# Kernel tuning notes

Measured on AMD Instinct MI355X. Metric: run time of the kernel, lower is better.

Reference implementation:

```python
import jax, jax.numpy as jnp
import numpy as np

N_EMBD = 1024
N_HEAD = 16
HEAD_DIM = N_EMBD // N_HEAD
BLOCK = 2048
BATCH = 2


def setup_inputs() -> dict:
    key = jax.random.key(0)
    ks = jax.random.split(key, 6)
    s_in = 1.0 / np.sqrt(N_EMBD)
    s_hd = 1.0 / np.sqrt(N_EMBD)  # fan-in of c_proj1 is n_head*head_dim = n_embd
    return {
        "x": jax.random.normal(ks[0], (BATCH, BLOCK, N_EMBD), jnp.float32),
        "wq": jax.random.normal(ks[1], (N_EMBD, N_HEAD, HEAD_DIM), jnp.float32) * s_in,
        "wk": jax.random.normal(ks[2], (N_EMBD, N_HEAD, HEAD_DIM), jnp.float32) * s_in,
        "wv": jax.random.normal(ks[3], (N_EMBD, N_HEAD, HEAD_DIM), jnp.float32) * s_in,
        "wp1": jax.random.normal(ks[4], (N_HEAD, HEAD_DIM, N_EMBD), jnp.float32) * s_hd,
        "wp2": jax.random.normal(ks[5], (N_EMBD, N_EMBD), jnp.float32) * s_in,
    }


def reference(x, wq, wk, wv, wp1, wp2):
    # QKV projections: DenseGeneral(features=(H, D), axis=-1), no bias
    q = jnp.einsum('btc,chd->bthd', x, wq)
    k = jnp.einsum('btc,chd->bthd', x, wk)
    v = jnp.einsum('btc,chd->bthd', x, wv)
    scale = HEAD_DIM ** (-0.5)
    wei = jnp.einsum('bqhd,bkhd->bhqk', q, k) * scale  # [B,H,T,T]
    tril = jnp.tril(jnp.ones((BLOCK, BLOCK), dtype=bool))
    wei = jnp.where(tril, wei, -jnp.inf)
    wei = jax.nn.softmax(wei, axis=-1)
    att = jnp.einsum('bhqk,bkhd->bqhd', wei, v)  # [B,T,H,D]
    # c_proj1: DenseGeneral over (-2,-1) -> contract (H,D)
    y = jnp.einsum('bqhd,hdc->bqc', att, wp1)
    # c_proj2: Dense
    out = jnp.einsum('bqc,ce->bqe', y, wp2)
    return out
```

## Files before the change

kernel.cpp:

```cpp
#include <hip/hip_runtime.h>
#include <hip/hip_bf16.h>
#include <stdint.h>

typedef __bf16 bf16;
typedef __bf16 bf16x4 __attribute__((ext_vector_type(4)));
typedef __bf16 bf16x8 __attribute__((ext_vector_type(8)));
typedef float  f32x4  __attribute__((ext_vector_type(4)));

#define MFMA16(a,b,c) __builtin_amdgcn_mfma_f32_16x16x32_bf16((a),(b),(c),0,0,0)

#define TSEQ 2048
#define NE   1024
#define NE3  3072
#define NH   16
#define HD   64
#define MTOK 4096

#if defined(__has_builtin)
#if __has_builtin(__builtin_amdgcn_exp2f)
#define EXP2F(x) __builtin_amdgcn_exp2f(x)
#else
#define EXP2F(x) exp2f(x)
#endif
#else
#define EXP2F(x) exp2f(x)
#endif

__device__ __forceinline__ void gl_lds16(const bf16* g, bf16* l) {
  __builtin_amdgcn_global_load_lds(
      (const __attribute__((address_space(1))) void*)g,
      (__attribute__((address_space(3))) void*)l,
      16, 0, 0);
}

__global__ void k_cast(const float* __restrict__ in, bf16* __restrict__ out, int n4) {
  int i = blockIdx.x * blockDim.x + threadIdx.x;
  if (i < n4) {
    float4 v = reinterpret_cast<const float4*>(in)[i];
    bf16x4 o = { (bf16)v.x, (bf16)v.y, (bf16)v.z, (bf16)v.w };
    reinterpret_cast<bf16x4*>(out)[i] = o;
  }
}

__global__ void k_transpose_all(const float* __restrict__ wq, const float* __restrict__ wk,
                                const float* __restrict__ wv, const float* __restrict__ wp1,
                                const float* __restrict__ wp2,
                                bf16* __restrict__ W3T, bf16* __restrict__ Wp1T,
                                bf16* __restrict__ Wp2T) {
  __shared__ float tile[64][65];
  const int z = blockIdx.z;
  const float* in = (z == 0) ? wq : (z == 1) ? wk : (z == 2) ? wv : (z == 3) ? wp1 : wp2;
  bf16* out = (z < 3) ? (W3T + (size_t)z * 1024 * 1024) : (z == 3 ? Wp1T : Wp2T);
  const int r0 = blockIdx.y * 64, c0 = blockIdx.x * 64;
  const int lc = threadIdx.x & 63, lr0 = threadIdx.x >> 6;
#pragma unroll
  for (int i = 0; i < 16; ++i) {
    int lr = i*4 + lr0;
    tile[lr][lc] = in[(size_t)(r0 + lr) * 1024 + (c0 + lc)];
  }
  __syncthreads();
#pragma unroll
  for (int i = 0; i < 16; ++i) {
    int lr = i*4 + lr0;
    out[(size_t)(c0 + lr) * 1024 + (r0 + lc)] = (bf16)tile[lc][lr];
  }
}

__global__ void k_transpose_v(const bf16* __restrict__ V, bf16* __restrict__ Vt) {
  __shared__ bf16 tile[64][65];
  const int b = blockIdx.z, h = blockIdx.y, t0 = blockIdx.x * 64;
  const int lc = threadIdx.x & 63, lr0 = threadIdx.x >> 6;
#pragma unroll
  for (int i = 0; i < 16; ++i) {
    int lr = i*4 + lr0;
    tile[lr][lc] = V[(size_t)(b*TSEQ + t0 + lr)*NE3 + h*HD + lc];
  }
  __syncthreads();
#pragma unroll
  for (int i = 0; i < 16; ++i) {
    int lr = i*4 + lr0;
    Vt[((size_t)(b*NH + h)*HD + lr)*TSEQ + t0 + lc] = tile[lc][lr];
  }
}

template<int BN, typename OutT>
__global__ __launch_bounds__(256) void k_gemm_bt(const bf16* __restrict__ A,
                                                 const bf16* __restrict__ Bt,
                                                 OutT* __restrict__ C,
                                                 const int M, const int N, const int K) {
  constexpr int NC = BN / 32;
  __shared__ bf16 As[2][128*32];
  __shared__ bf16 Bs[2][BN*32];
  const int tid  = threadIdx.x;
  const int lane = tid & 63;
  const int wave = tid >> 6;
  const int wr = (wave >> 1) * 64;
  const int wc = (wave & 1) * (BN/2);
  const int l15 = lane & 15;
  const int l4  = lane >> 4;
  const int bm = blockIdx.y * 128;
  const int bn = blockIdx.x * BN;

  const int srow = tid >> 2;
  const int scol = ((tid & 3) ^ ((tid >> 3) & 3)) * 8;
  const bf16* ag = A  + (size_t)(bm + srow) * K + scol;
  const bf16* bg = Bt + (size_t)(bn + srow) * K + scol;
  const int kx = (l4 ^ ((l15 >> 1) & 3)) * 8;

  f32x4 acc[4][NC] = {};

  auto stage = [&](int buf, int k0) {
    bf16* al = As[buf] + tid * 8;
    bf16* bl = Bs[buf] + tid * 8;
    gl_lds16(ag + k0,                   al);
    gl_lds16(ag + k0 + (size_t)64 * K,  al + 64*32);
    gl_lds16(bg + k0,                   bl);
    if (BN == 128) gl_lds16(bg + k0 + (size_t)64 * K, bl + 64*32);
  };

  stage(0, 0);
  __syncthreads();
  int cur = 0;
  for (int k0 = 0; k0 < K; k0 += 32) {
    if (k0 + 32 < K) stage(cur ^ 1, k0 + 32);
    bf16x8 af[4], bfr[NC];
#pragma unroll
    for (int m = 0; m < 4; ++m)
      af[m] = *reinterpret_cast<const bf16x8*>(&As[cur][(wr + m*16 + l15)*32 + kx]);
#pragma unroll
    for (int n = 0; n < NC; ++n)
      bfr[n] = *reinterpret_cast<const bf16x8*>(&Bs[cur][(wc + n*16 + l15)*32 + kx]);
#pragma unroll
    for (int m = 0; m < 4; ++m)
#pragma unroll
      for (int n = 0; n < NC; ++n)
        acc[m][n] = MFMA16(af[m], bfr[n], acc[m][n]);
    __syncthreads();
    cur ^= 1;
  }

#pragma unroll
  for (int m = 0; m < 4; ++m) {
    const int row = bm + wr + m*16 + l4*4;
#pragma unroll
    for (int n = 0; n < NC; ++n) {
      const int col = bn + wc + n*16 + l15;
#pragma unroll
      for (int r = 0; r < 4; ++r)
        C[(size_t)(row + r) * N + col] = (OutT)acc[m][n][r];
    }
  }
}

__global__ __launch_bounds__(256) void k_attn(const bf16* __restrict__ QKV,
                                              const bf16* __restrict__ Vt,
                                              bf16* __restrict__ O) {
  __shared__ bf16 Ks[2][2*64*32];
  __shared__ bf16 Vs[2][2*64*32];
  __shared__ bf16 Ps[4][2*32*32];

  const int tid  = threadIdx.x;
  const int lane = tid & 63;
  const int wave = tid >> 6;
  const int l15 = lane & 15;
  const int l4  = lane >> 4;

  const int x  = blockIdx.x;
  const int qb = 15 - (x >> 5);
  const int bh = x & 31;
  const int b  = bh >> 4, h = bh & 15;
  const int qw = qb * 128 + wave * 32;
  const int nt = 2 * qb + 2;

  const bf16* Qb = QKV + (size_t)b*TSEQ*NE3 +        h*HD;
  const bf16* Kb = QKV + (size_t)b*TSEQ*NE3 + 1024 + h*HD;
  const bf16* Vb = Vt  + (size_t)bh*HD*TSEQ;
  bf16* Pw = Ps[wave];

  const float SC = 0.125f * 1.44269504f;
  bf16x8 qf[2][2];
#pragma unroll
  for (int qi = 0; qi < 2; ++qi)
#pragma unroll
    for (int ks = 0; ks < 2; ++ks) {
      bf16x8 qv = *reinterpret_cast<const bf16x8*>(
          &Qb[(size_t)(qw + qi*16 + l15)*NE3 + ks*32 + l4*8]);
#pragma unroll
      for (int j = 0; j < 8; ++j) qv[j] = (bf16)((float)qv[j] * SC);
      qf[qi][ks] = qv;
    }

  f32x4 ot[2][4] = {};
  float m_run[2] = {-1e30f, -1e30f};
  float l_part[2] = {0.f, 0.f};

  const int srow = tid >> 2;
  const int sg   = ((tid & 3) ^ ((tid >> 3) & 3));
  const int swz  = (l4 ^ ((l15 >> 1) & 3)) * 8;

  auto stage = [&](int buf, int t) {
#pragma unroll
    for (int ks = 0; ks < 2; ++ks)
      gl_lds16(&Kb[(size_t)(t*64 + srow)*NE3 + ks*32 + sg*8], &Ks[buf][ks*2048 + tid*8]);
#pragma unroll
    for (int ks = 0; ks < 2; ++ks)
      gl_lds16(&Vb[(size_t)srow*TSEQ + t*64 + ks*32 + sg*8],  &Vs[buf][ks*2048 + tid*8]);
  };

  stage(0, 0);
  __syncthreads();
  int cur = 0;

  for (int t = 0; t < nt; ++t) {
    if (t + 1 < nt) stage(cur ^ 1, t + 1);

    if (t*64 <= qw + 31) {
      f32x4 st[2][4] = {};
#pragma unroll
      for (int kvf = 0; kvf < 4; ++kvf) {
        const int row = kvf*16 + l15;
#pragma unroll
        for (int ks = 0; ks < 2; ++ks) {
          bf16x8 kf = *reinterpret_cast<const bf16x8*>(&Ks[cur][ks*2048 + row*32 + swz]);
          st[0][kvf] = MFMA16(kf, qf[0][ks], st[0][kvf]);
          st[1][kvf] = MFMA16(kf, qf[1][ks], st[1][kvf]);
        }
      }

      const bool maskNeeded = (t*64 + 63 > qw);
#pragma unroll
      for (int qi = 0; qi < 2; ++qi) {
        const int q = qw + qi*16 + l15;
        if (maskNeeded) {
#pragma unroll
          for (int kvf = 0; kvf < 4; ++kvf)
#pragma unroll
            for (int r = 0; r < 4; ++r)
              if (t*64 + kvf*16 + l4*4 + r > q) st[qi][kvf][r] = -1e30f;
        }
        float mx = st[qi][0][0];
#pragma unroll
        for (int kvf = 0; kvf < 4; ++kvf)
#pragma unroll
          for (int r = 0; r < 4; ++r) mx = fmaxf(mx, st[qi][kvf][r]);
        mx = fmaxf(mx, __shfl_xor(mx, 16));
        mx = fmaxf(mx, __shfl_xor(mx, 32));

        if (__any(mx > m_run[qi] + 8.f)) {
          const float mnew = fmaxf(m_run[qi], mx);
          const float corr = EXP2F(m_run[qi] - mnew);
          l_part[qi] *= corr;
#pragma unroll
          for (int n2 = 0; n2 < 4; ++n2) ot[qi][n2] *= corr;
          m_run[qi] = mnew;
        }

        float rs = 0.f;
#pragma unroll
        for (int kvf = 0; kvf < 4; ++kvf) {
          bf16x4 pk;
#pragma unroll
          for (int r = 0; r < 4; ++r) {
            const float p = EXP2F(st[qi][kvf][r] - m_run[qi]);
            rs += p;
            pk[r] = (bf16)p;
          }
          const int gp = (((kvf & 1)*2 + (l4 >> 1)) ^ ((l15 >> 1) & 3));
          *reinterpret_cast<bf16x4*>(
              &Pw[(kvf>>1)*1024 + (qi*16 + l15)*32 + gp*8 + (l4 & 1)*4]) = pk;
        }
        l_part[qi] += rs;
      }

      bf16x8 pa[2][2];
#pragma unroll
      for (int qi = 0; qi < 2; ++qi)
#pragma unroll
        for (int ks = 0; ks < 2; ++ks)
          pa[qi][ks] = *reinterpret_cast<const bf16x8*>(
              &Pw[ks*1024 + (qi*16 + l15)*32 + swz]);
#pragma unroll
      for (int n2 = 0; n2 < 4; ++n2) {
        const int vrow = n2*16 + l15;
#pragma unroll
        for (int ks = 0; ks < 2; ++ks) {
          bf16x8 vf = *reinterpret_cast<const bf16x8*>(&Vs[cur][ks*2048 + vrow*32 + swz]);
          ot[0][n2] = MFMA16(vf, pa[0][ks], ot[0][n2]);
          ot[1][n2] = MFMA16(vf, pa[1][ks], ot[1][n2]);
        }
      }
    }

    __syncthreads();
    cur ^= 1;
  }

#pragma unroll
  for (int qi = 0; qi < 2; ++qi) {
    float l = l_part[qi];
    l += __shfl_xor(l, 16);
    l += __shfl_xor(l, 32);
    const float rl = 1.f / l;
    const size_t row = (size_t)(b*TSEQ + qw + qi*16 + l15);
#pragma unroll
    for (int n2 = 0; n2 < 4; ++n2) {
      bf16x4 ov;
#pragma unroll
      for (int r = 0; r < 4; ++r) ov[r] = (bf16)(ot[qi][n2][r] * rl);
      *reinterpret_cast<bf16x4*>(&O[row*NE + h*HD + n2*16 + l4*4]) = ov;
    }
  }
}

extern "C" void kernel_launch(void* const* d_in, const int* in_sizes, int n_in,
                              void* d_out, int out_size, void* d_ws, size_t ws_size,
                              hipStream_t stream) {
  const float* x   = (const float*)d_in[0];
  const float* wq  = (const float*)d_in[1];
  const float* wk  = (const float*)d_in[2];
  const float* wv  = (const float*)d_in[3];
  const float* wp1 = (const float*)d_in[4];
  const float* wp2 = (const float*)d_in[5];
  float* out = (float*)d_out;

  char* ws = (char*)d_ws;
  const size_t MB = 1024ull * 1024ull;
  bf16* xb   = (bf16*)(ws + 0*MB);
  bf16* W3T  = (bf16*)(ws + 8*MB);
  bf16* wp1T = (bf16*)(ws + 14*MB);
  bf16* wp2T = (bf16*)(ws + 16*MB);
  bf16* QKVb = (bf16*)(ws + 18*MB);
  bf16* Vtb  = (bf16*)(ws + 42*MB);
  bf16* attb = (bf16*)(ws + 50*MB);
  bf16* yb   = (bf16*)(ws + 58*MB);

  k_cast<<<4096, 256, 0, stream>>>(x, xb, MTOK*NE/4);
  k_transpose_all<<<dim3(16, 16, 5), 256, 0, stream>>>(wq, wk, wv, wp1, wp2,
                                                       W3T, wp1T, wp2T);

  k_gemm_bt<128, bf16><<<dim3(24, 32), 256, 0, stream>>>(xb, W3T, QKVb, MTOK, NE3, NE);

  k_transpose_v<<<dim3(TSEQ/64, NH, 2), 256, 0, stream>>>(QKVb + 2048, Vtb);

  k_attn<<<dim3(512), 256, 0, stream>>>(QKVb, Vtb, attb);

  k_gemm_bt<64, bf16 ><<<dim3(16, 32), 256, 0, stream>>>(attb, wp1T, yb,  MTOK, NE, NE);
  k_gemm_bt<64, float><<<dim3(16, 32), 256, 0, stream>>>(yb,   wp2T, out, MTOK, NE, NE);
}
```

Baseline: 142.3 us.

## Fold output projections into one weight, rebalance causal attention, swizzle GEMM tiles

Precomputes the product of the two output projection weights on device, so the attention output needs one GEMM instead of two. Attention blocks shrink to two waves, and each block handles a paired short and long causal chunk so work per block evens out. GEMM tiles are remapped in groups of eight to improve cache locality. The exp2 builtin is swapped for exp2f. Folding the weights adds a small 1024^3 GEMM per call and changes bf16 rounding.

```diff
diff --git a/kernel.cpp b/kernel.cpp
--- a/kernel.cpp
+++ b/kernel.cpp
@@ -16,15 +16,7 @@
 #define HD   64
 #define MTOK 4096
 
-#if defined(__has_builtin)
-#if __has_builtin(__builtin_amdgcn_exp2f)
-#define EXP2F(x) __builtin_amdgcn_exp2f(x)
-#else
 #define EXP2F(x) exp2f(x)
-#endif
-#else
-#define EXP2F(x) exp2f(x)
-#endif
 
 __device__ __forceinline__ void gl_lds16(const bf16* g, bf16* l) {
   __builtin_amdgcn_global_load_lds(
@@ -43,14 +35,12 @@
 }
 
 __global__ void k_transpose_all(const float* __restrict__ wq, const float* __restrict__ wk,
-                                const float* __restrict__ wv, const float* __restrict__ wp1,
-                                const float* __restrict__ wp2,
-                                bf16* __restrict__ W3T, bf16* __restrict__ Wp1T,
-                                bf16* __restrict__ Wp2T) {
+                                const float* __restrict__ wv, const float* __restrict__ wp2,
+                                bf16* __restrict__ W3T, bf16* __restrict__ Wp2T) {
   __shared__ float tile[64][65];
   const int z = blockIdx.z;
-  const float* in = (z == 0) ? wq : (z == 1) ? wk : (z == 2) ? wv : (z == 3) ? wp1 : wp2;
-  bf16* out = (z < 3) ? (W3T + (size_t)z * 1024 * 1024) : (z == 3 ? Wp1T : Wp2T);
+  const float* in = (z == 0) ? wq : (z == 1) ? wk : (z == 2) ? wv : wp2;
+  bf16* out = (z < 3) ? (W3T + (size_t)z * 1024 * 1024) : Wp2T;
   const int r0 = blockIdx.y * 64, c0 = blockIdx.x * 64;
   const int lc = threadIdx.x & 63, lr0 = threadIdx.x >> 6;
 #pragma unroll
@@ -98,8 +88,12 @@
   const int wc = (wave & 1) * (BN/2);
   const int l15 = lane & 15;
   const int l4  = lane >> 4;
-  const int bm = blockIdx.y * 128;
-  const int bn = blockIdx.x * BN;
+
+  const int nwg = gridDim.x * gridDim.y;
+  int id = blockIdx.y * gridDim.x + blockIdx.x;
+  id = (id & 7) * (nwg >> 3) + (id >> 3);
+  const int bm = (id / gridDim.x) * 128;
+  const int bn = (id % gridDim.x) * BN;
 
   const int srow = tid >> 2;
   const int scol = ((tid & 3) ^ ((tid >> 3) & 3)) * 8;
@@ -152,12 +146,12 @@
   }
 }
 
-__global__ __launch_bounds__(256) void k_attn(const bf16* __restrict__ QKV,
+__global__ __launch_bounds__(128) void k_attn(const bf16* __restrict__ QKV,
                                               const bf16* __restrict__ Vt,
                                               bf16* __restrict__ O) {
   __shared__ bf16 Ks[2][2*64*32];
   __shared__ bf16 Vs[2][2*64*32];
-  __shared__ bf16 Ps[4][2*32*32];
+  __shared__ bf16 Ps[2][2*32*32];
 
   const int tid  = threadIdx.x;
   const int lane = tid & 63;
@@ -166,11 +160,9 @@
   const int l4  = lane >> 4;
 
   const int x  = blockIdx.x;
-  const int qb = 15 - (x >> 5);
+  const int p  = x >> 5;
   const int bh = x & 31;
   const int b  = bh >> 4, h = bh & 15;
-  const int qw = qb * 128 + wave * 32;
-  const int nt = 2 * qb + 2;
 
   const bf16* Qb = QKV + (size_t)b*TSEQ*NE3 +        h*HD;
   const bf16* Kb = QKV + (size_t)b*TSEQ*NE3 + 1024 + h*HD;
@@ -178,43 +170,62 @@
   bf16* Pw = Ps[wave];
 
   const float SC = 0.125f * 1.44269504f;
-  bf16x8 qf[2][2];
-#pragma unroll
-  for (int qi = 0; qi < 2; ++qi)
-#pragma unroll
-    for (int ks = 0; ks < 2; ++ks) {
-      bf16x8 qv = *reinterpret_cast<const bf16x8*>(
-          &Qb[(size_t)(qw + qi*16 + l15)*NE3 + ks*32 + l4*8]);
-#pragma unroll
-      for (int j = 0; j < 8; ++j) qv[j] = (bf16)((float)qv[j] * SC);
-      qf[qi][ks] = qv;
-    }
-
-  f32x4 ot[2][4] = {};
-  float m_run[2] = {-1e30f, -1e30f};
-  float l_part[2] = {0.f, 0.f};
-
-  const int srow = tid >> 2;
-  const int sg   = ((tid & 3) ^ ((tid >> 3) & 3));
-  const int swz  = (l4 ^ ((l15 >> 1) & 3)) * 8;
+  const int swz = (l4 ^ ((l15 >> 1) & 3)) * 8;
+  const int sr = tid >> 2;
+  const int sg = tid & 3;
 
   auto stage = [&](int buf, int t) {
 #pragma unroll
     for (int ks = 0; ks < 2; ++ks)
-      gl_lds16(&Kb[(size_t)(t*64 + srow)*NE3 + ks*32 + sg*8], &Ks[buf][ks*2048 + tid*8]);
+#pragma unroll
+      for (int half = 0; half < 2; ++half) {
+        const int r = half*32 + sr;
+        const int g = sg ^ ((r >> 1) & 3);
+        gl_lds16(&Kb[(size_t)(t*64 + r)*NE3 + ks*32 + g*8],
+                 &Ks[buf][ks*2048 + half*1024 + tid*8]);
+      }
 #pragma unroll
     for (int ks = 0; ks < 2; ++ks)
-      gl_lds16(&Vb[(size_t)srow*TSEQ + t*64 + ks*32 + sg*8],  &Vs[buf][ks*2048 + tid*8]);
+#pragma unroll
+      for (int half = 0; half < 2; ++half) {
+        const int r = half*32 + sr;
+        const int g = sg ^ ((r >> 1) & 3);
+        gl_lds16(&Vb[(size_t)r*TSEQ + t*64 + ks*32 + g*8],
+                 &Vs[buf][ks*2048 + half*1024 + tid*8]);
+      }
   };
 
   stage(0, 0);
   __syncthreads();
   int cur = 0;
-
-  for (int t = 0; t < nt; ++t) {
-    if (t + 1 < nt) stage(cur ^ 1, t + 1);
-
-    if (t*64 <= qw + 31) {
+  int i = 0;
+
+  for (int ci = 0; ci < 2; ++ci) {
+    const int c  = ci ? (31 - p) : p;
+    const int qw = c*64 + wave*32;
+
+    bf16x8 qf[2][2];
+#pragma unroll
+    for (int qi = 0; qi < 2; ++qi)
+#pragma unroll
+      for (int ks = 0; ks < 2; ++ks) {
+        bf16x8 qv = *reinterpret_cast<const bf16x8*>(
+            &Qb[(size_t)(qw + qi*16 + l15)*NE3 + ks*32 + l4*8]);
+#pragma unroll
+        for (int j = 0; j < 8; ++j) qv[j] = (bf16)((float)qv[j] * SC);
+        qf[qi][ks] = qv;
+      }
+
+    f32x4 ot[2][4] = {};
+    float m_run[2] = {-1e30f, -1e30f};
+    float l_part[2] = {0.f, 0.f};
+
+    for (int t = 0; t <= c; ++t, ++i) {
+      if (i + 1 < 33) {
+        const int nt2 = (i + 1 <= p) ? (i + 1) : (i - p);
+        stage(cur ^ 1, nt2);
+      }
+
       f32x4 st[2][4] = {};
 #pragma unroll
       for (int kvf = 0; kvf < 4; ++kvf) {
@@ -261,9 +272,9 @@
           bf16x4 pk;
 #pragma unroll
           for (int r = 0; r < 4; ++r) {
-            const float p = EXP2F(st[qi][kvf][r] - m_run[qi]);
-            rs += p;
-            pk[r] = (bf16)p;
+            const float pv = EXP2F(st[qi][kvf][r] - m_run[qi]);
+            rs += pv;
+            pk[r] = (bf16)pv;
           }
           const int gp = (((kvf & 1)*2 + (l4 >> 1)) ^ ((l15 >> 1) & 3));
           *reinterpret_cast<bf16x4*>(
@@ -289,25 +300,25 @@
           ot[1][n2] = MFMA16(vf, pa[1][ks], ot[1][n2]);
         }
       }
+
+      __syncthreads();
+      cur ^= 1;
     }
 
-    __syncthreads();
-    cur ^= 1;
-  }
-
-#pragma unroll
-  for (int qi = 0; qi < 2; ++qi) {
-    float l = l_part[qi];
-    l += __shfl_xor(l, 16);
-    l += __shfl_xor(l, 32);
-    const float rl = 1.f / l;
-    const size_t row = (size_t)(b*TSEQ + qw + qi*16 + l15);
-#pragma unroll
-    for (int n2 = 0; n2 < 4; ++n2) {
-      bf16x4 ov;
-#pragma unroll
-      for (int r = 0; r < 4; ++r) ov[r] = (bf16)(ot[qi][n2][r] * rl);
-      *reinterpret_cast<bf16x4*>(&O[row*NE + h*HD + n2*16 + l4*4]) = ov;
+#pragma unroll
+    for (int qi = 0; qi < 2; ++qi) {
+      float l = l_part[qi];
+      l += __shfl_xor(l, 16);
+      l += __shfl_xor(l, 32);
+      const float rl = 1.f / l;
+      const size_t row = (size_t)(b*TSEQ + qw + qi*16 + l15);
+#pragma unroll
+      for (int n2 = 0; n2 < 4; ++n2) {
+        bf16x4 ov;
+#pragma unroll
+        for (int r = 0; r < 4; ++r) ov[r] = (bf16)(ot[qi][n2][r] * rl);
+        *reinterpret_cast<bf16x4*>(&O[row*NE + h*HD + n2*16 + l4*4]) = ov;
+      }
     }
   }
 }
@@ -327,23 +338,24 @@
   const size_t MB = 1024ull * 1024ull;
   bf16* xb   = (bf16*)(ws + 0*MB);
   bf16* W3T  = (bf16*)(ws + 8*MB);
-  bf16* wp1T = (bf16*)(ws + 14*MB);
+  bf16* wp1b = (bf16*)(ws + 14*MB);
   bf16* wp2T = (bf16*)(ws + 16*MB);
-  bf16* QKVb = (bf16*)(ws + 18*MB);
-  bf16* Vtb  = (bf16*)(ws + 42*MB);
-  bf16* attb = (bf16*)(ws + 50*MB);
-  bf16* yb   = (bf16*)(ws + 58*MB);
+  bf16* WcT  = (bf16*)(ws + 18*MB);
+  bf16* QKVb = (bf16*)(ws + 20*MB);
+  bf16* Vtb  = (bf16*)(ws + 44*MB);
+  bf16* attb = (bf16*)(ws + 52*MB);
 
   k_cast<<<4096, 256, 0, stream>>>(x, xb, MTOK*NE/4);
-  k_transpose_all<<<dim3(16, 16, 5), 256, 0, stream>>>(wq, wk, wv, wp1, wp2,
-                                                       W3T, wp1T, wp2T);
+  k_cast<<<1024, 256, 0, stream>>>(wp1, wp1b, 1024*1024/4);
+  k_transpose_all<<<dim3(16, 16, 4), 256, 0, stream>>>(wq, wk, wv, wp2, W3T, wp2T);
+
+  k_gemm_bt<128, bf16><<<dim3(8, 8), 256, 0, stream>>>(wp2T, wp1b, WcT, 1024, 1024, 1024);
 
   k_gemm_bt<128, bf16><<<dim3(24, 32), 256, 0, stream>>>(xb, W3T, QKVb, MTOK, NE3, NE);
 
   k_transpose_v<<<dim3(TSEQ/64, NH, 2), 256, 0, stream>>>(QKVb + 2048, Vtb);
 
-  k_attn<<<dim3(512), 256, 0, stream>>>(QKVb, Vtb, attb);
-
-  k_gemm_bt<64, bf16 ><<<dim3(16, 32), 256, 0, stream>>>(attb, wp1T, yb,  MTOK, NE, NE);
-  k_gemm_bt<64, float><<<dim3(16, 32), 256, 0, stream>>>(yb,   wp2T, out, MTOK, NE, NE);
-}
+  k_attn<<<dim3(512), 128, 0, stream>>>(QKVb, Vtb, attb);
+
+  k_gemm_bt<128, float><<<dim3(8, 32), 256, 0, stream>>>(attb, WcT, out, MTOK, NE, NE);
+}
```

New measurement: 178.9 us. 25.7% more time.
